# Performance work log

Hardware: AMD Instinct MI355X
Metric: run time of the kernel (lower is better)

Reference implementation:

```python
import jax, jax.numpy as jnp
import numpy as np

EMBED_DIM = 768
NUM_HEADS = 12
HEAD_DIM = EMBED_DIM // NUM_HEADS
B, T = 2, 2048


def setup_inputs() -> dict:
    key = jax.random.key(0)
    kx, kq, kqb, ko, kob = jax.random.split(key, 5)
    x = jax.random.normal(kx, (B, T, EMBED_DIM), dtype=jnp.float32)
    # xavier-uniform style params
    lim_qkv = float(np.sqrt(6.0 / (EMBED_DIM + 3 * EMBED_DIM)))
    qkv_kernel = jax.random.uniform(kq, (EMBED_DIM, 3 * EMBED_DIM), minval=-lim_qkv, maxval=lim_qkv, dtype=jnp.float32)
    qkv_bias = jnp.zeros((3 * EMBED_DIM,), dtype=jnp.float32)
    lim_o = float(np.sqrt(6.0 / (EMBED_DIM + EMBED_DIM)))
    o_kernel = jax.random.uniform(ko, (EMBED_DIM, EMBED_DIM), minval=-lim_o, maxval=lim_o, dtype=jnp.float32)
    o_bias = jnp.zeros((EMBED_DIM,), dtype=jnp.float32)
    return {"x": x, "qkv_kernel": qkv_kernel, "qkv_bias": qkv_bias, "o_kernel": o_kernel, "o_bias": o_bias}


def reference(x, qkv_kernel, qkv_bias, o_kernel, o_bias):
    b, t, d = x.shape
    # fused QKV projection
    qkv = jnp.einsum('btd,de->bte', x, qkv_kernel) + qkv_bias  # [B,T,3D]
    qkv = qkv.reshape(b, t, 3, NUM_HEADS, HEAD_DIM).transpose(2, 0, 3, 1, 4)  # [3,B,H,T,Dh]
    q, k, v = qkv[0], qkv[1], qkv[2]
    # naive attention: materializes full [B,H,T,T] scores (as in original)
    scale = 1.0 / np.sqrt(HEAD_DIM).astype(np.float32)
    attn_logits = jnp.einsum('bhqd,bhkd->bhqk', q, k) * scale
    attention = jax.nn.softmax(attn_logits, axis=-1)
    values = jnp.einsum('bhqk,bhkd->bhqd', attention, v)
    values = values.transpose(0, 2, 1, 3).reshape(b, t, d)  # [B,T,D]
    o = jnp.einsum('btd,de->bte', values, o_kernel) + o_bias
    return (o, attention)
```

## Files before the change

kernel.cpp:

```cpp
#include <hip/hip_runtime.h>
#include <hip/hip_bf16.h>
#include <hip/hip_fp16.h>

typedef _Float16 f16;
typedef _Float16 f16x4 __attribute__((ext_vector_type(4)));
typedef _Float16 f16x8 __attribute__((ext_vector_type(8)));
typedef float f32x4 __attribute__((ext_vector_type(4)));

#define MFMA16(a, b, c) __builtin_amdgcn_mfma_f32_16x16x32_f16(a, b, c, 0, 0, 0)

__device__ __forceinline__ float fexp2(float x) {
#if __has_builtin(__builtin_amdgcn_exp2f)
    return __builtin_amdgcn_exp2f(x);
#else
    return exp2f(x);
#endif
}

typedef __attribute__((address_space(1))) const void gconst_t;
typedef __attribute__((address_space(3))) void lds_t;
__device__ __forceinline__ void gload16(const f16* g, f16* l) {
    __builtin_amdgcn_global_load_lds((gconst_t*)g, (lds_t*)l, 16, 0, 0);
}

__global__ void k_convert_x(const float* __restrict__ in, f16* __restrict__ out, int n4) {
    int i = blockIdx.x * blockDim.x + threadIdx.x;
    if (i >= n4) return;
    float4 v = ((const float4*)in)[i];
    f16x4 o = {(f16)v.x, (f16)v.y, (f16)v.z, (f16)v.w};
    ((f16x4*)out)[i] = o;
}

__global__ __launch_bounds__(256) void k_transpose(const float* __restrict__ in,
                                                   f16* __restrict__ out, int K, int N) {
    __shared__ f16 tile[64][72];
    int n0 = blockIdx.x * 64, k0 = blockIdx.y * 64;
    int t = threadIdx.x;
    int r = t >> 2, cb = (t & 3) * 16;
    const float* src = in + (size_t)(k0 + r) * N + n0 + cb;
#pragma unroll
    for (int j = 0; j < 4; ++j) {
        float4 v = ((const float4*)src)[j];
        tile[r][cb + 4 * j + 0] = (f16)v.x;
        tile[r][cb + 4 * j + 1] = (f16)v.y;
        tile[r][cb + 4 * j + 2] = (f16)v.z;
        tile[r][cb + 4 * j + 3] = (f16)v.w;
    }
    __syncthreads();
    int nl = t >> 2, kb = (t & 3) * 16;
    f16* dst = out + (size_t)(n0 + nl) * K + k0 + kb;
#pragma unroll
    for (int j = 0; j < 2; ++j) {
        f16x8 o;
#pragma unroll
        for (int e = 0; e < 8; ++e) o[e] = tile[kb + 8 * j + e][nl];
        *(f16x8*)(dst + 8 * j) = o;
    }
}

__device__ __forceinline__ void gemm_core(const f16* __restrict__ A, const f16* __restrict__ Bt,
                                          int m0, int n0, int lane, int w, int wr, int wc,
                                          f16* As, f16* Bs, f32x4 acc[4][4]) {
    int prow = lane >> 2, pc = lane & 3;
    int lrow = prow ^ ((prow >> 2) & 1);
    int lcol = (pc ^ (lrow & 3)) * 8;
    int rsw = (lane & 7) << 3;
    for (int kt = 0; kt < 24; ++kt) {
        const f16* ab = A + (size_t)(m0 + w * 32 + lrow) * 768 + kt * 32 + lcol;
        const f16* bb = Bt + (size_t)(n0 + w * 32 + lrow) * 768 + kt * 32 + lcol;
        gload16(ab, As + (w * 32) * 32);
        gload16(ab + (size_t)16 * 768, As + (w * 32 + 16) * 32);
        gload16(bb, Bs + (w * 32) * 32);
        gload16(bb + (size_t)16 * 768, Bs + (w * 32 + 16) * 32);
        __syncthreads();
        f16x8 a[4], b[4];
#pragma unroll
        for (int i = 0; i < 4; ++i) {
            int idx = (wr * 64 + i * 16 + (lane & 15)) * 32 + (lane >> 4) * 8;
            a[i] = *(const f16x8*)(As + (idx ^ rsw));
        }
#pragma unroll
        for (int j = 0; j < 4; ++j) {
            int idx = (wc * 64 + j * 16 + (lane & 15)) * 32 + (lane >> 4) * 8;
            b[j] = *(const f16x8*)(Bs + (idx ^ rsw));
        }
#pragma unroll
        for (int i = 0; i < 4; ++i)
#pragma unroll
            for (int j = 0; j < 4; ++j) acc[i][j] = MFMA16(a[i], b[j], acc[i][j]);
        __syncthreads();
    }
}

__global__ __launch_bounds__(256) void k_qkv_gemm(const f16* __restrict__ A, const f16* __restrict__ Bt,
                                                  const float* __restrict__ bias,
                                                  f16* __restrict__ Qh, f16* __restrict__ Kf,
                                                  f16* __restrict__ Vf) {
    __shared__ __align__(16) f16 As[128 * 32];
    __shared__ __align__(16) f16 Bs[128 * 32];
    int m0 = blockIdx.x * 128, n0 = blockIdx.y * 128;
    int t = threadIdx.x, lane = t & 63, w = t >> 6;
    int wr = w >> 1, wc = w & 1;
    f32x4 zero = {0.f, 0.f, 0.f, 0.f};
    f32x4 acc[4][4];
#pragma unroll
    for (int i = 0; i < 4; ++i)
#pragma unroll
        for (int j = 0; j < 4; ++j) acc[i][j] = zero;

    gemm_core(A, Bt, m0, n0, lane, w, wr, wc, As, Bs, acc);

    const float QSCALE = 0.18033688011112042f;
#pragma unroll
    for (int j = 0; j < 4; ++j) {
        int n = n0 + wc * 64 + j * 16 + (lane & 15);
        int which = n / 768;
        int rem = n - which * 768;
        int h = rem >> 6, d = rem & 63;
        float bv = bias[n];
#pragma unroll
        for (int i = 0; i < 4; ++i) {
            int m = m0 + wr * 64 + i * 16 + ((lane >> 4) << 2);
            int bb = m >> 11, tt = m & 2047;
            int bh = bb * 12 + h;
            if (which == 2) {
                int kt = tt >> 6;
                int half = (tt & 63) >> 5, hi = (tt & 31) >> 3, e0 = tt & 7;
                int jd = d >> 4, lo = d & 15;
                size_t addr = (((size_t)bh * 32 + kt) * 8 + jd * 2 + half) * 512 +
                              (size_t)(hi * 16 + lo) * 8 + e0;
                f16x4 pk;
#pragma unroll
                for (int r = 0; r < 4; ++r) pk[r] = (f16)(acc[i][j][r] + bv);
                *(f16x4*)(Vf + addr) = pk;
            } else if (which == 0) {
#pragma unroll
                for (int r = 0; r < 4; ++r)
                    Qh[((size_t)bh * 2048 + tt + r) * 64 + d] = (f16)((acc[i][j][r] + bv) * QSCALE);
            } else {
                int half = d >> 5, hi = (d & 31) >> 3, e = d & 7;
#pragma unroll
                for (int r = 0; r < 4; ++r) {
                    int tr = tt + r;
                    int kt = tr >> 6, row = tr & 63;
                    int s = row >> 4, lo = row & 15;
                    size_t addr = (((size_t)bh * 32 + kt) * 8 + s * 2 + half) * 512 +
                                  (size_t)(hi * 16 + lo) * 8 + e;
                    Kf[addr] = (f16)(acc[i][j][r] + bv);
                }
            }
        }
    }
}

__global__ __launch_bounds__(256) void k_o_gemm(const f16* __restrict__ A, const f16* __restrict__ Bt,
                                                const float* __restrict__ bias,
                                                float* __restrict__ out) {
    __shared__ __align__(16) f16 As[128 * 32];
    __shared__ __align__(16) f16 Bs[128 * 32];
    int m0 = blockIdx.x * 128, n0 = blockIdx.y * 128;
    int t = threadIdx.x, lane = t & 63, w = t >> 6;
    int wr = w >> 1, wc = w & 1;
    f32x4 zero = {0.f, 0.f, 0.f, 0.f};
    f32x4 acc[4][4];
#pragma unroll
    for (int i = 0; i < 4; ++i)
#pragma unroll
        for (int j = 0; j < 4; ++j) acc[i][j] = zero;

    gemm_core(A, Bt, m0, n0, lane, w, wr, wc, As, Bs, acc);

#pragma unroll
    for (int j = 0; j < 4; ++j) {
        int n = n0 + wc * 64 + j * 16 + (lane & 15);
        float bv = bias[n];
#pragma unroll
        for (int i = 0; i < 4; ++i) {
            int m = m0 + wr * 64 + i * 16 + ((lane >> 4) << 2);
#pragma unroll
            for (int r = 0; r < 4; ++r) out[(size_t)(m + r) * 768 + n] = acc[i][j][r] + bv;
        }
    }
}

__global__ __launch_bounds__(256) void k_lsum(const f16* __restrict__ Qh, const f16* __restrict__ Kf,
                                              float* __restrict__ lpart) {
    int qt = blockIdx.x, bh = blockIdx.y, kc = blockIdx.z;
    int q0 = qt * 64;
    int t = threadIdx.x, lane = t & 63, w = t >> 6;
    const f16* qbase = Qh + ((size_t)bh * 2048 + q0 + w * 16) * 64;
    const f16* kfb = Kf + (size_t)bh * 32 * 4096 + (size_t)lane * 8;

    f16x8 aq[2];
#pragma unroll
    for (int f = 0; f < 2; ++f)
        aq[f] = *(const f16x8*)(qbase + (size_t)(lane & 15) * 64 + f * 32 + (lane >> 4) * 8);
    f32x4 zero = {0.f, 0.f, 0.f, 0.f};

    auto LOADK = [&](f16x8* dst, int kt) {
        const f16* kp = kfb + (size_t)kt * 4096;
#pragma unroll
        for (int f = 0; f < 8; ++f) dst[f] = *(const f16x8*)(kp + f * 512);
    };
    auto QKTS = [&](const f16x8* kf, f32x4* s4) {
#pragma unroll
        for (int s = 0; s < 4; ++s) {
            s4[s] = MFMA16(kf[2 * s], aq[0], zero);
            s4[s] = MFMA16(kf[2 * s + 1], aq[1], s4[s]);
        }
    };

    f16x8 ka[8], kb2[8];
    float lsum = 0.f;
    int base = kc * 8;
    LOADK(ka, base);
    for (int i = 0; i < 8; i += 2) {
        f32x4 s4[4];
        LOADK(kb2, base + i + 1);
        QKTS(ka, s4);
#pragma unroll
        for (int s = 0; s < 4; ++s)
#pragma unroll
            for (int r = 0; r < 4; ++r) lsum += fexp2(s4[s][r]);
        LOADK(ka, base + ((i + 2) & 7));
        QKTS(kb2, s4);
#pragma unroll
        for (int s = 0; s < 4; ++s)
#pragma unroll
            for (int r = 0; r < 4; ++r) lsum += fexp2(s4[s][r]);
    }
    lsum += __shfl_xor(lsum, 16, 64);
    lsum += __shfl_xor(lsum, 32, 64);
    float* lp = lpart + (size_t)kc * 49152 + (size_t)bh * 2048 + q0 + w * 16;
    if (lane < 16) lp[lane] = lsum;
}

__global__ __launch_bounds__(256, 3) void k_attn(const f16* __restrict__ Qh, const f16* __restrict__ Kf,
                                                 const f16* __restrict__ Vf,
                                                 const float* __restrict__ lpart,
                                                 float* __restrict__ attn, f16* __restrict__ valh) {
    __shared__ __align__(16) float Ps32_all[4][16 * 68];
    int orig = blockIdx.x;
    int swz = (orig & 7) * 96 + (orig >> 3);
    int bh = swz >> 5, qt = swz & 31;
    int q0 = qt * 64;
    int t = threadIdx.x, lane = t & 63, w = t >> 6;

    const f16* qbase = Qh + ((size_t)bh * 2048 + q0 + w * 16) * 64;
    const f16* kfb = Kf + (size_t)bh * 32 * 4096 + (size_t)lane * 8;
    const f16* vfb = Vf + (size_t)bh * 32 * 4096 + (size_t)lane * 8;

    f16x8 aq[2];
#pragma unroll
    for (int f = 0; f < 2; ++f)
        aq[f] = *(const f16x8*)(qbase + (size_t)(lane & 15) * 64 + f * 32 + (lane >> 4) * 8);
    f32x4 zero = {0.f, 0.f, 0.f, 0.f};

    float linv;
    {
        size_t qoff = (size_t)bh * 2048 + q0 + w * 16 + (lane & 15);
        float s = 0.f;
#pragma unroll
        for (int kc = 0; kc < 4; ++kc) s += lpart[(size_t)kc * 49152 + qoff];
        linv = 1.0f / s;
    }

    auto LOADK = [&](f16x8* dst, int kt) {
        const f16* kp = kfb + (size_t)kt * 4096;
#pragma unroll
        for (int f = 0; f < 8; ++f) dst[f] = *(const f16x8*)(kp + f * 512);
    };
    auto QKTS = [&](const f16x8* kf, f32x4* s4) {
#pragma unroll
        for (int s = 0; s < 4; ++s) {
            s4[s] = MFMA16(kf[2 * s], aq[0], zero);
            s4[s] = MFMA16(kf[2 * s + 1], aq[1], s4[s]);
        }
    };

    f32x4 accv[4];
#pragma unroll
    for (int j = 0; j < 4; ++j) accv[j] = zero;
    float* Ps = Ps32_all[w];
    float* attn_base = attn + ((size_t)bh * 2048 + q0 + w * 16) * 2048;
    f16x8 ka[8], kb2[8], vbuf[8];

    auto step2 = [&](f16x8* curK, f16x8* nxtK, int kt) {
        {
            const f16* vp = vfb + (size_t)kt * 4096;
#pragma unroll
            for (int f = 0; f < 8; ++f) vbuf[f] = *(const f16x8*)(vp + f * 512);
        }
        LOADK(nxtK, (kt + 1) & 31);
        f32x4 s4[4];
        QKTS(curK, s4);
#pragma unroll
        for (int s = 0; s < 4; ++s) {
            f32x4 pv;
#pragma unroll
            for (int r = 0; r < 4; ++r) pv[r] = fexp2(s4[s][r]) * linv;
            *(f32x4*)(Ps + (lane & 15) * 68 + s * 16 + (lane >> 4) * 4) = pv;
        }
        f16x8 pa[2];
#pragma unroll
        for (int half = 0; half < 2; ++half) {
            const float* pr = Ps + (lane & 15) * 68 + half * 32 + (lane >> 4) * 8;
            f32x4 lo = *(const f32x4*)(pr);
            f32x4 hi = *(const f32x4*)(pr + 4);
            f16x8 pf = {(f16)lo[0], (f16)lo[1], (f16)lo[2], (f16)lo[3],
                        (f16)hi[0], (f16)hi[1], (f16)hi[2], (f16)hi[3]};
            pa[half] = pf;
        }
        float* ab = attn_base + kt * 64;
#pragma unroll
        for (int i = 0; i < 4; ++i) {
            int row = i * 4 + (lane >> 4);
            int col = (lane & 15) * 4;
            f32x4 v = *(const f32x4*)(Ps + row * 68 + col);
            *(f32x4*)(ab + (size_t)row * 2048 + col) = v;
        }
#pragma unroll
        for (int jd = 0; jd < 4; ++jd) {
            accv[jd] = MFMA16(pa[0], vbuf[2 * jd], accv[jd]);
            accv[jd] = MFMA16(pa[1], vbuf[2 * jd + 1], accv[jd]);
        }
    };

    LOADK(ka, 0);
    for (int kt = 0; kt < 32; kt += 2) {
        step2(ka, kb2, kt);
        step2(kb2, ka, kt + 1);
    }

    int b = bh / 12, h = bh - b * 12;
#pragma unroll
    for (int j = 0; j < 4; ++j) {
#pragma unroll
        for (int r = 0; r < 4; ++r) {
            int rowg = b * 2048 + q0 + w * 16 + (lane >> 4) * 4 + r;
            int col = h * 64 + j * 16 + (lane & 15);
            valh[(size_t)rowg * 768 + col] = (f16)accv[j][r];
        }
    }
}

extern "C" void kernel_launch(void* const* d_in, const int* in_sizes, int n_in,
                              void* d_out, int out_size, void* d_ws, size_t ws_size,
                              hipStream_t stream) {
    const float* x = (const float*)d_in[0];
    const float* wqkv = (const float*)d_in[1];
    const float* bqkv = (const float*)d_in[2];
    const float* wo = (const float*)d_in[3];
    const float* bo = (const float*)d_in[4];

    float* out_o = (float*)d_out;
    float* out_attn = out_o + (size_t)2 * 2048 * 768;

    f16* ws = (f16*)d_ws;
    f16* xh = ws;
    f16* wqkv_t = xh + 3145728;
    f16* wo_t = wqkv_t + 1769472;
    f16* Qh = wo_t + 589824;
    f16* Kf = Qh + 3145728;
    f16* Vf = Kf + 3145728;
    f16* valh = Vf + 3145728;
    float* lpart = (float*)(valh + 3145728);

    k_convert_x<<<3072, 256, 0, stream>>>(x, xh, 786432);
    k_transpose<<<dim3(36, 12), 256, 0, stream>>>(wqkv, wqkv_t, 768, 2304);
    k_transpose<<<dim3(12, 12), 256, 0, stream>>>(wo, wo_t, 768, 768);
    k_qkv_gemm<<<dim3(32, 18), 256, 0, stream>>>(xh, wqkv_t, bqkv, Qh, Kf, Vf);
    k_lsum<<<dim3(32, 24, 4), 256, 0, stream>>>(Qh, Kf, lpart);
    k_attn<<<768, 256, 0, stream>>>(Qh, Kf, Vf, lpart, out_attn, valh);
    k_o_gemm<<<dim3(32, 6), 256, 0, stream>>>(valh, wo_t, bo, out_o);
}
```

Baseline: 203.2 us.

## Split attention key range across two waves per query tile and reduce via LDS

Each 64-query attention block now runs 8 waves instead of 4, and each pair of waves splits the 32 key tiles into two halves. The second wave writes its partial PV accumulator to shared memory and the first adds it before storing the f16 values. The K double-buffer is dropped for a single buffer reloaded after the QK MFMAs, which lowers register pressure to allow 512-thread blocks. This doubles in-flight waves to better hide memory latency on the large attention-matrix writes, at the cost of an extra LDS reduction, a block barrier, and less prefetch distance per wave.

```diff
diff --git a/kernel.cpp b/kernel.cpp
--- a/kernel.cpp
+++ b/kernel.cpp
@@ -235,18 +235,19 @@
     if (lane < 16) lp[lane] = lsum;
 }
 
-__global__ __launch_bounds__(256, 3) void k_attn(const f16* __restrict__ Qh, const f16* __restrict__ Kf,
+__global__ __launch_bounds__(512, 4) void k_attn(const f16* __restrict__ Qh, const f16* __restrict__ Kf,
                                                  const f16* __restrict__ Vf,
                                                  const float* __restrict__ lpart,
                                                  float* __restrict__ attn, f16* __restrict__ valh) {
-    __shared__ __align__(16) float Ps32_all[4][16 * 68];
+    __shared__ __align__(16) float Ps32_all[8][16 * 68];
     int orig = blockIdx.x;
     int swz = (orig & 7) * 96 + (orig >> 3);
     int bh = swz >> 5, qt = swz & 31;
     int q0 = qt * 64;
     int t = threadIdx.x, lane = t & 63, w = t >> 6;
-
-    const f16* qbase = Qh + ((size_t)bh * 2048 + q0 + w * 16) * 64;
+    int qg = w >> 1, half = w & 1;
+
+    const f16* qbase = Qh + ((size_t)bh * 2048 + q0 + qg * 16) * 64;
     const f16* kfb = Kf + (size_t)bh * 32 * 4096 + (size_t)lane * 8;
     const f16* vfb = Vf + (size_t)bh * 32 * 4096 + (size_t)lane * 8;
 
@@ -258,7 +259,7 @@
 
     float linv;
     {
-        size_t qoff = (size_t)bh * 2048 + q0 + w * 16 + (lane & 15);
+        size_t qoff = (size_t)bh * 2048 + q0 + qg * 16 + (lane & 15);
         float s = 0.f;
 #pragma unroll
         for (int kc = 0; kc < 4; ++kc) s += lpart[(size_t)kc * 49152 + qoff];
@@ -270,30 +271,29 @@
 #pragma unroll
         for (int f = 0; f < 8; ++f) dst[f] = *(const f16x8*)(kp + f * 512);
     };
-    auto QKTS = [&](const f16x8* kf, f32x4* s4) {
-#pragma unroll
-        for (int s = 0; s < 4; ++s) {
-            s4[s] = MFMA16(kf[2 * s], aq[0], zero);
-            s4[s] = MFMA16(kf[2 * s + 1], aq[1], s4[s]);
-        }
-    };
 
     f32x4 accv[4];
 #pragma unroll
     for (int j = 0; j < 4; ++j) accv[j] = zero;
     float* Ps = Ps32_all[w];
-    float* attn_base = attn + ((size_t)bh * 2048 + q0 + w * 16) * 2048;
-    f16x8 ka[8], kb2[8], vbuf[8];
-
-    auto step2 = [&](f16x8* curK, f16x8* nxtK, int kt) {
+    float* attn_base = attn + ((size_t)bh * 2048 + q0 + qg * 16) * 2048;
+    f16x8 ka[8], vbuf[8];
+
+    int ktbase = half * 16;
+    LOADK(ka, ktbase);
+    for (int kt = ktbase; kt < ktbase + 16; ++kt) {
         {
             const f16* vp = vfb + (size_t)kt * 4096;
 #pragma unroll
             for (int f = 0; f < 8; ++f) vbuf[f] = *(const f16x8*)(vp + f * 512);
         }
-        LOADK(nxtK, (kt + 1) & 31);
         f32x4 s4[4];
-        QKTS(curK, s4);
+#pragma unroll
+        for (int s = 0; s < 4; ++s) {
+            s4[s] = MFMA16(ka[2 * s], aq[0], zero);
+            s4[s] = MFMA16(ka[2 * s + 1], aq[1], s4[s]);
+        }
+        LOADK(ka, (kt + 1) & 31);
 #pragma unroll
         for (int s = 0; s < 4; ++s) {
             f32x4 pv;
@@ -303,13 +303,13 @@
         }
         f16x8 pa[2];
 #pragma unroll
-        for (int half = 0; half < 2; ++half) {
-            const float* pr = Ps + (lane & 15) * 68 + half * 32 + (lane >> 4) * 8;
+        for (int hh = 0; hh < 2; ++hh) {
+            const float* pr = Ps + (lane & 15) * 68 + hh * 32 + (lane >> 4) * 8;
             f32x4 lo = *(const f32x4*)(pr);
             f32x4 hi = *(const f32x4*)(pr + 4);
             f16x8 pf = {(f16)lo[0], (f16)lo[1], (f16)lo[2], (f16)lo[3],
                         (f16)hi[0], (f16)hi[1], (f16)hi[2], (f16)hi[3]};
-            pa[half] = pf;
+            pa[hh] = pf;
         }
         float* ab = attn_base + kt * 64;
 #pragma unroll
@@ -324,22 +324,28 @@
             accv[jd] = MFMA16(pa[0], vbuf[2 * jd], accv[jd]);
             accv[jd] = MFMA16(pa[1], vbuf[2 * jd + 1], accv[jd]);
         }
-    };
-
-    LOADK(ka, 0);
-    for (int kt = 0; kt < 32; kt += 2) {
-        step2(ka, kb2, kt);
-        step2(kb2, ka, kt + 1);
-    }
-
-    int b = bh / 12, h = bh - b * 12;
-#pragma unroll
-    for (int j = 0; j < 4; ++j) {
-#pragma unroll
-        for (int r = 0; r < 4; ++r) {
-            int rowg = b * 2048 + q0 + w * 16 + (lane >> 4) * 4 + r;
-            int col = h * 64 + j * 16 + (lane & 15);
-            valh[(size_t)rowg * 768 + col] = (f16)accv[j][r];
+    }
+
+    if (half) {
+#pragma unroll
+        for (int j = 0; j < 4; ++j)
+#pragma unroll
+            for (int r = 0; r < 4; ++r)
+                Ps[((lane >> 4) * 4 + r) * 68 + j * 16 + (lane & 15)] = accv[j][r];
+    }
+    __syncthreads();
+    if (!half) {
+        const float* Pp = Ps32_all[w + 1];
+        int b = bh / 12, h = bh - b * 12;
+#pragma unroll
+        for (int j = 0; j < 4; ++j) {
+#pragma unroll
+            for (int r = 0; r < 4; ++r) {
+                float v = accv[j][r] + Pp[((lane >> 4) * 4 + r) * 68 + j * 16 + (lane & 15)];
+                int rowg = b * 2048 + q0 + qg * 16 + (lane >> 4) * 4 + r;
+                int col = h * 64 + j * 16 + (lane & 15);
+                valh[(size_t)rowg * 768 + col] = (f16)v;
+            }
         }
     }
 }
@@ -371,6 +377,6 @@
     k_transpose<<<dim3(12, 12), 256, 0, stream>>>(wo, wo_t, 768, 768);
     k_qkv_gemm<<<dim3(32, 18), 256, 0, stream>>>(xh, wqkv_t, bqkv, Qh, Kf, Vf);
     k_lsum<<<dim3(32, 24, 4), 256, 0, stream>>>(Qh, Kf, lpart);
-    k_attn<<<768, 256, 0, stream>>>(Qh, Kf, Vf, lpart, out_attn, valh);
+    k_attn<<<768, 512, 0, stream>>>(Qh, Kf, Vf, lpart, out_attn, valh);
     k_o_gemm<<<dim3(32, 6), 256, 0, stream>>>(valh, wo_t, bo, out_o);
 }
```

After: 200.0 us. No clear change (-1.6%).
